# Performance work log

Hardware: AMD Instinct MI355X
Metric: run time of the kernel (lower is better)

## Reference

```python
import jax, jax.numpy as jnp
import numpy as np

BETA = 0.25
K = 1024   # codebook_size
D = 64     # emb_dim


def setup_inputs() -> dict:
    key = jax.random.key(0)
    k1, k2 = jax.random.split(key)
    z_e = jax.random.normal(k1, (32, 64, 64, D), dtype=jnp.float32)
    codebook = jax.random.normal(k2, (K, D), dtype=jnp.float32) * 0.05
    return {"z_e": z_e, "codebook": codebook}


def reference(z_e, codebook):
    sg = jax.lax.stop_gradient
    k, d = codebook.shape
    z = z_e.reshape(-1, d)                                   # [N, D]
    # squared euclidean distances: ||z||^2 + ||e||^2 - 2 z.e
    z_sq = jnp.sum(z * z, axis=1, keepdims=True)             # [N, 1]
    e_sq = jnp.sum(codebook * codebook, axis=1)              # [K]
    distances = z_sq + e_sq[None, :] - 2.0 * (z @ codebook.T)  # [N, K]
    indices = jnp.argmin(distances, axis=1)                  # [N] int
    z_q = jnp.take(codebook, indices, axis=0).reshape(z_e.shape)
    commitment = jnp.mean((sg(z_e) - z_q) ** 2)
    codebook_loss = jnp.mean((z_e - sg(z_q)) ** 2)
    z_q_st = z_e + sg(z_q - z_e)
    loss_vq = codebook_loss + BETA * commitment
    # perplexity (no-grad in original)
    n = z.shape[0]
    counts = jnp.zeros((k,), dtype=jnp.float32).at[indices].add(1.0)
    avg_probs = sg(counts / n)
    perplexity = jnp.exp(-jnp.sum(avg_probs * jnp.log(avg_probs + 1e-12)))
    return z_q_st, indices.reshape(z_e.shape[:-1]), loss_vq, perplexity
```

## Files before the change

kernel.cpp:

```cpp
#include <hip/hip_runtime.h>

#define N_VEC   131072
#define D       64
#define KCODES  1024
#define NT      64
#define BLK     256
#define VPB     128
#define CH      4
#define NCH     (NT / CH)

typedef __attribute__((ext_vector_type(8))) short bf16x8;
typedef __attribute__((ext_vector_type(4))) float f32x4;

#define GLD16(dst, src) __builtin_amdgcn_global_load_lds(                      \
    (const __attribute__((address_space(1))) void*)(src),                      \
    (__attribute__((address_space(3))) void*)(dst), 16, 0, 0)


__device__ __forceinline__ float4 f4fma(float4 a, float4 b, float4 c) {
    return make_float4(fmaf(a.x, b.x, c.x), fmaf(a.y, b.y, c.y),
                       fmaf(a.z, b.z, c.z), fmaf(a.w, b.w, c.w));
}
__device__ __forceinline__ float f4rsum(float4 a) {
    return (a.x + a.y) + (a.z + a.w);
}
__device__ __forceinline__ unsigned short f2bf(float f) {
    union { float f; unsigned u; } x; x.f = f;
    unsigned r = x.u + 0x7FFFu + ((x.u >> 16) & 1u);
    return (unsigned short)(r >> 16);
}
__device__ __forceinline__ float bf2f(unsigned short h) {
    union { unsigned u; float f; } x; x.u = ((unsigned)h) << 16;
    return x.f;
}
__device__ __forceinline__ int   f_as_i(float f) { union { float f; int i; } x; x.f = f; return x.i; }
__device__ __forceinline__ float i_as_f(int i)   { union { int i; float f; } x; x.i = i; return x.f; }

__global__ void prep_kernel(const float* __restrict__ cb, float* __restrict__ esq,
                            bf16x8* __restrict__ afrag, float4* __restrict__ efrag) {
    __shared__ float sesq[64];
    const int tid = threadIdx.x;
    const int c0  = blockIdx.x * 64;
    if (tid < 64) {
        const float4* c4 = reinterpret_cast<const float4*>(cb + (size_t)(c0 + tid) * D);
        float4 p = make_float4(0.f, 0.f, 0.f, 0.f);
        #pragma unroll
        for (int i = 0; i < 16; ++i) { float4 v = c4[i]; p = f4fma(v, v, p); }
        float e = f4rsum(p);
        esq[c0 + tid] = e;
        sesq[tid] = e;
    }
    __syncthreads();
    const int tt = tid >> 6;
    const int L  = tid & 63;
    const int t  = blockIdx.x * 4 + tt;
    const int g  = L >> 4;
    const int r  = t * 16 + (L & 15);
    #pragma unroll
    for (int ks = 0; ks < 2; ++ks) {
        const float* src = cb + (size_t)r * D + ks * 32 + g * 8;
        bf16x8 h, l;
        #pragma unroll
        for (int e = 0; e < 8; ++e) {
            float f = src[e];
            unsigned short hb = f2bf(f);
            float lo = f - bf2f(hb);
            h[e] = (short)hb;
            l[e] = (short)f2bf(lo);
        }
        afrag[(t * 4 + ks * 2 + 0) * 64 + L] = h;
        afrag[(t * 4 + ks * 2 + 1) * 64 + L] = l;
    }
    float4 ef;
    ef.x = sesq[tt * 16 + g * 4 + 0];
    ef.y = sesq[tt * 16 + g * 4 + 1];
    ef.z = sesq[tt * 16 + g * 4 + 2];
    ef.w = sesq[tt * 16 + g * 4 + 3];
    efrag[t * 64 + L] = ef;
}

__device__ __forceinline__ void insd(float ov, int og,
                                     float& v0, float& v1, float& v2,
                                     int& g0, int& g1, int& g2) {
    bool b1 = (ov > v0) || (ov == v0 && og < g0);
    bool b2 = (ov > v1) || (ov == v1 && og < g1);
    bool b3 = (ov > v2) || (ov == v2 && og < g2);
    float nv2 = b2 ? v1 : (b3 ? ov : v2);
    int   ng2 = b2 ? g1 : (b3 ? og : g2);
    float nv1 = b1 ? v0 : (b2 ? ov : v1);
    int   ng1 = b1 ? g0 : (b2 ? og : g1);
    v0 = b1 ? ov : v0;
    g0 = b1 ? og : g0;
    v1 = nv1; g1 = ng1; v2 = nv2; g2 = ng2;
}

__launch_bounds__(BLK)
__global__ void vq_fused(const float* __restrict__ z_e, const float* __restrict__ cb,
                         const float* __restrict__ esq,
                         const float4* __restrict__ afrag4, const float4* __restrict__ efrag,
                         float* __restrict__ zq_out, float* __restrict__ idx_out,
                         float* __restrict__ sse, int* __restrict__ counts) {
    __shared__ float4 scb[2][CH * 4 * 64];
    __shared__ float4 sef[2][CH * 64];
    char* ovl = (char*)&scb[0][0];
    int  (*scand)[3] = reinterpret_cast<int(*)[3]>(ovl);
    float* sZsq = reinterpret_cast<float*>(ovl + 2048);
    float* sS1  = reinterpret_cast<float*>(ovl + 2560);
    float* sS2  = reinterpret_cast<float*>(ovl + 3072);
    float* sC2  = reinterpret_cast<float*>(ovl + 3584);
    float* sred = reinterpret_cast<float*>(ovl + 4096);

    const int tid  = threadIdx.x;
    const int wave = tid >> 6;
    const int L    = tid & 63;
    const int lrow = L & 15;
    const int g    = L >> 4;
    const size_t vbase = (size_t)blockIdx.x * VPB + wave * 32;

    bf16x8 zhi[2][2], zlo[2][2];
    #pragma unroll
    for (int b = 0; b < 2; ++b) {
        #pragma unroll
        for (int ks = 0; ks < 2; ++ks) {
            const float* zp = z_e + (vbase + b * 16 + lrow) * D + ks * 32 + g * 8;
            float4 u0 = *reinterpret_cast<const float4*>(zp);
            float4 u1 = *reinterpret_cast<const float4*>(zp + 4);
            float fv[8] = {u0.x, u0.y, u0.z, u0.w, u1.x, u1.y, u1.z, u1.w};
            bf16x8 h, l;
            #pragma unroll
            for (int e = 0; e < 8; ++e) {
                unsigned short hb = f2bf(fv[e]);
                float lo = fv[e] - bf2f(hb);
                h[e] = (short)hb;
                l[e] = (short)f2bf(lo);
            }
            zhi[b][ks] = h; zlo[b][ks] = l;
        }
    }

    float m1[2], m2[2], m3[2];
    #pragma unroll
    for (int b = 0; b < 2; ++b) { m1[b] = m2[b] = m3[b] = -INFINITY; }

    #pragma unroll
    for (int i = 0; i < 4; ++i) GLD16(&scb[0][i * BLK + tid], afrag4 + i * BLK + tid);
    GLD16(&sef[0][tid], efrag + tid);

    int cur = 0;
    for (int c = 0; c < NCH; ++c) {
        __syncthreads();
        if (c + 1 < NCH) {
            const float4* gA = afrag4 + (size_t)(c + 1) * (CH * 4 * 64);
            const float4* gE = efrag + (size_t)(c + 1) * (CH * 64);
            #pragma unroll
            for (int i = 0; i < 4; ++i) GLD16(&scb[cur ^ 1][i * BLK + tid], gA + i * BLK + tid);
            GLD16(&sef[cur ^ 1][tid], gE + tid);
        }

        #pragma unroll
        for (int tt = 0; tt < CH; ++tt) {
            const int tglob = c * CH + tt;
            const bf16x8* fr = reinterpret_cast<const bf16x8*>(&scb[cur][tt * 256]);
            bf16x8 Ah0 = fr[0 * 64 + L];
            bf16x8 Al0 = fr[1 * 64 + L];
            bf16x8 Ah1 = fr[2 * 64 + L];
            bf16x8 Al1 = fr[3 * 64 + L];
            float4 ef  = sef[cur][tt * 64 + L];

            #pragma unroll
            for (int b = 0; b < 2; ++b) {
                f32x4 aA = (f32x4){0.f, 0.f, 0.f, 0.f};
                f32x4 aB = (f32x4){0.f, 0.f, 0.f, 0.f};
                aA = __builtin_amdgcn_mfma_f32_16x16x32_bf16(Ah0, zhi[b][0], aA, 0, 0, 0);
                aB = __builtin_amdgcn_mfma_f32_16x16x32_bf16(Ah0, zlo[b][0], aB, 0, 0, 0);
                aB = __builtin_amdgcn_mfma_f32_16x16x32_bf16(Al0, zhi[b][0], aB, 0, 0, 0);
                aA = __builtin_amdgcn_mfma_f32_16x16x32_bf16(Ah1, zhi[b][1], aA, 0, 0, 0);
                aB = __builtin_amdgcn_mfma_f32_16x16x32_bf16(Ah1, zlo[b][1], aB, 0, 0, 0);
                aB = __builtin_amdgcn_mfma_f32_16x16x32_bf16(Al1, zhi[b][1], aB, 0, 0, 0);

                #pragma unroll
                for (int j = 0; j < 4; ++j) {
                    float ej = (j == 0) ? ef.x : (j == 1) ? ef.y : (j == 2) ? ef.z : ef.w;
                    float s = fmaf(2.0f, aA[j], fmaf(2.0f, aB[j], -ej));
                    int komp = 255 - ((tglob << 2) | j);
                    float pd = i_as_f((f_as_i(s) & 0xFFFFFF00) | komp);
                    float t1 = fminf(m1[b], pd); m1[b] = fmaxf(m1[b], pd);
                    float t2 = fminf(m2[b], t1); m2[b] = fmaxf(m2[b], t1);
                    m3[b] = fmaxf(m3[b], t2);
                }
            }
        }
        cur ^= 1;
    }

    __syncthreads();

    #pragma unroll
    for (int b = 0; b < 2; ++b) {
        float v0, v1, v2; int g0, g1, g2;
        {
            int p0 = f_as_i(m1[b]), p1 = f_as_i(m2[b]), p2 = f_as_i(m3[b]);
            int c0 = 255 - (p0 & 255), c1 = 255 - (p1 & 255), c2 = 255 - (p2 & 255);
            v0 = i_as_f(p0 & ~255); g0 = (c0 >> 2) * 16 + g * 4 + (c0 & 3);
            v1 = i_as_f(p1 & ~255); g1 = (c1 >> 2) * 16 + g * 4 + (c1 & 3);
            v2 = i_as_f(p2 & ~255); g2 = (c2 >> 2) * 16 + g * 4 + (c2 & 3);
        }
        #pragma unroll
        for (int m = 16; m <= 32; m <<= 1) {
            float ov0 = __shfl_xor(v0, m), ov1 = __shfl_xor(v1, m), ov2 = __shfl_xor(v2, m);
            int   og0 = __shfl_xor(g0, m), og1 = __shfl_xor(g1, m), og2 = __shfl_xor(g2, m);
            insd(ov0, og0, v0, v1, v2, g0, g1, g2);
            insd(ov1, og1, v0, v1, v2, g0, g1, g2);
            insd(ov2, og2, v0, v1, v2, g0, g1, g2);
        }
        if (g == 0) {
            int lv = wave * 32 + b * 16 + lrow;
            scand[lv][0] = g0; scand[lv][1] = g1; scand[lv][2] = g2;
        }
    }
    __syncthreads();

    const int vid = tid & (VPB - 1);
    const int sub = tid >> 7;
    const size_t n = (size_t)blockIdx.x * VPB + vid;
    {
        const float4* z4 = reinterpret_cast<const float4*>(z_e + n * D);
        if (sub == 0) {
            int ci0 = scand[vid][0];
            const float4* cp0 = reinterpret_cast<const float4*>(cb + (size_t)ci0 * D);
            float4 pq = make_float4(0.f, 0.f, 0.f, 0.f);
            float4 s0 = pq;
            #pragma unroll
            for (int i = 0; i < 16; ++i) {
                float4 zz = z4[i];
                pq = f4fma(zz, zz, pq);
                s0 = f4fma(zz, cp0[i], s0);
            }
            sZsq[vid] = f4rsum(pq);
            sS1[vid]  = f4rsum(s0);
        } else {
            int ci1 = scand[vid][1];
            int ci2 = scand[vid][2];
            const float4* cp1 = reinterpret_cast<const float4*>(cb + (size_t)ci1 * D);
            const float4* cp2 = reinterpret_cast<const float4*>(cb + (size_t)ci2 * D);
            float4 s1 = make_float4(0.f, 0.f, 0.f, 0.f);
            float4 s2 = s1;
            #pragma unroll
            for (int i = 0; i < 16; ++i) {
                float4 zz = z4[i];
                s1 = f4fma(zz, cp1[i], s1);
                s2 = f4fma(zz, cp2[i], s2);
            }
            sS2[vid] = f4rsum(s1);
            sC2[vid] = f4rsum(s2);
        }
    }
    __syncthreads();

    float v = 0.f;
    if (sub == 0) {
        int ci0 = scand[vid][0], ci1 = scand[vid][1], ci2 = scand[vid][2];
        float zsq = sZsq[vid];
        float d0 = fmaf(-2.0f, sS1[vid], zsq + esq[ci0]);
        float d1 = fmaf(-2.0f, sS2[vid], zsq + esq[ci1]);
        float d2 = fmaf(-2.0f, sC2[vid], zsq + esq[ci2]);
        float bd = d0; int bi = ci0;
        if (d1 < bd || (d1 == bd && ci1 < bi)) { bd = d1; bi = ci1; }
        if (d2 < bd || (d2 == bd && ci2 < bi)) { bd = d2; bi = ci2; }
        idx_out[n] = (float)bi;
        atomicAdd(&counts[bi], 1);
        scand[vid][0] = bi;
        v = bd;
    }
    #pragma unroll
    for (int off = 32; off > 0; off >>= 1) v += __shfl_down(v, off);
    if ((tid & 63) == 0) sred[tid >> 6] = v;
    __syncthreads();
    if (tid == 0) atomicAdd(sse, (sred[0] + sred[1]) + (sred[2] + sred[3]));

    const float4* cb4 = reinterpret_cast<const float4*>(cb);
    float4* zq4 = reinterpret_cast<float4*>(zq_out) + (size_t)blockIdx.x * (VPB * 16);
    #pragma unroll
    for (int i = 0; i < 8; ++i) {
        int mi  = i * BLK + tid;
        int vec = mi >> 4;
        int e   = mi & 15;
        zq4[mi] = cb4[(size_t)scand[vec][0] * 16 + e];
    }
}

__global__ void finalize_kernel(const int* __restrict__ counts, const float* __restrict__ sse,
                                float* __restrict__ out_loss, float* __restrict__ out_perp) {
    __shared__ float red[256];
    int tid = threadIdx.x;
    float hsum = 0.f;
    for (int k = tid; k < KCODES; k += 256) {
        float p = (float)counts[k] / (float)N_VEC;
        hsum += p * logf(p + 1e-12f);
    }
    red[tid] = hsum;
    __syncthreads();
    for (int s = 128; s > 0; s >>= 1) {
        if (tid < s) red[tid] += red[tid + s];
        __syncthreads();
    }
    if (tid == 0) {
        out_loss[0] = 1.25f * sse[0] / 8388608.0f;
        out_perp[0] = expf(-red[0]);
    }
}

extern "C" void kernel_launch(void* const* d_in, const int* in_sizes, int n_in,
                              void* d_out, int out_size, void* d_ws, size_t ws_size,
                              hipStream_t stream) {
    const float* z_e = (const float*)d_in[0];
    const float* cb  = (const float*)d_in[1];

    float* out  = (float*)d_out;
    float* zq   = out;
    float* idxo = out + (size_t)N_VEC * D;
    float* loss = idxo + N_VEC;
    float* perp = loss + 1;

    char* ws = (char*)d_ws;
    int*    counts = (int*)ws;
    float*  sse    = (float*)(ws + 4096);
    float*  esq    = (float*)(ws + 5120);
    float4* efrag  = (float4*)(ws + 16384);
    bf16x8* afrag  = (bf16x8*)(ws + 81920);

    hipMemsetAsync(d_ws, 0, 5120, stream);
    prep_kernel<<<16, 256, 0, stream>>>(cb, esq, afrag, efrag);
    vq_fused<<<N_VEC / VPB, BLK, 0, stream>>>(z_e, cb, esq, (const float4*)afrag, efrag,
                                              zq, idxo, sse, counts);
    finalize_kernel<<<1, 256, 0, stream>>>(counts, sse, loss, perp);
}
```

Baseline: 106.0 us.

## Load codebook fragments directly from global into registers with prefetch, drop LDS staging

```diff
diff --git a/kernel.cpp b/kernel.cpp
--- a/kernel.cpp
+++ b/kernel.cpp
@@ -6,15 +6,9 @@
 #define NT      64
 #define BLK     256
 #define VPB     128
-#define CH      4
-#define NCH     (NT / CH)
 
 typedef __attribute__((ext_vector_type(8))) short bf16x8;
 typedef __attribute__((ext_vector_type(4))) float f32x4;
-
-#define GLD16(dst, src) __builtin_amdgcn_global_load_lds(                      \
-    (const __attribute__((address_space(1))) void*)(src),                      \
-    (__attribute__((address_space(3))) void*)(dst), 16, 0, 0)
 
 
 __device__ __forceinline__ float4 f4fma(float4 a, float4 b, float4 c) {
@@ -97,18 +91,15 @@
 __launch_bounds__(BLK)
 __global__ void vq_fused(const float* __restrict__ z_e, const float* __restrict__ cb,
                          const float* __restrict__ esq,
-                         const float4* __restrict__ afrag4, const float4* __restrict__ efrag,
+                         const bf16x8* __restrict__ afragv, const float4* __restrict__ efrag,
                          float* __restrict__ zq_out, float* __restrict__ idx_out,
                          float* __restrict__ sse, int* __restrict__ counts) {
-    __shared__ float4 scb[2][CH * 4 * 64];
-    __shared__ float4 sef[2][CH * 64];
-    char* ovl = (char*)&scb[0][0];
-    int  (*scand)[3] = reinterpret_cast<int(*)[3]>(ovl);
-    float* sZsq = reinterpret_cast<float*>(ovl + 2048);
-    float* sS1  = reinterpret_cast<float*>(ovl + 2560);
-    float* sS2  = reinterpret_cast<float*>(ovl + 3072);
-    float* sC2  = reinterpret_cast<float*>(ovl + 3584);
-    float* sred = reinterpret_cast<float*>(ovl + 4096);
+    __shared__ int   scand[VPB][3];
+    __shared__ float sZsq[VPB];
+    __shared__ float sS1[VPB];
+    __shared__ float sS2[VPB];
+    __shared__ float sC2[VPB];
+    __shared__ float sred[4];
 
     const int tid  = threadIdx.x;
     const int wave = tid >> 6;
@@ -142,58 +133,48 @@
     #pragma unroll
     for (int b = 0; b < 2; ++b) { m1[b] = m2[b] = m3[b] = -INFINITY; }
 
-    #pragma unroll
-    for (int i = 0; i < 4; ++i) GLD16(&scb[0][i * BLK + tid], afrag4 + i * BLK + tid);
-    GLD16(&sef[0][tid], efrag + tid);
-
-    int cur = 0;
-    for (int c = 0; c < NCH; ++c) {
-        __syncthreads();
-        if (c + 1 < NCH) {
-            const float4* gA = afrag4 + (size_t)(c + 1) * (CH * 4 * 64);
-            const float4* gE = efrag + (size_t)(c + 1) * (CH * 64);
+    bf16x8 nAh0 = afragv[0 * 64 + L];
+    bf16x8 nAl0 = afragv[1 * 64 + L];
+    bf16x8 nAh1 = afragv[2 * 64 + L];
+    bf16x8 nAl1 = afragv[3 * 64 + L];
+    float4 nef  = efrag[L];
+
+    #pragma unroll 2
+    for (int t = 0; t < NT; ++t) {
+        bf16x8 Ah0 = nAh0, Al0 = nAl0, Ah1 = nAh1, Al1 = nAl1;
+        float4 ef  = nef;
+        if (t + 1 < NT) {
+            const bf16x8* np = afragv + (size_t)(t + 1) * 256;
+            nAh0 = np[0 * 64 + L];
+            nAl0 = np[1 * 64 + L];
+            nAh1 = np[2 * 64 + L];
+            nAl1 = np[3 * 64 + L];
+            nef  = efrag[(size_t)(t + 1) * 64 + L];
+        }
+
+        #pragma unroll
+        for (int b = 0; b < 2; ++b) {
+            f32x4 aA = (f32x4){0.f, 0.f, 0.f, 0.f};
+            f32x4 aB = (f32x4){0.f, 0.f, 0.f, 0.f};
+            aA = __builtin_amdgcn_mfma_f32_16x16x32_bf16(Ah0, zhi[b][0], aA, 0, 0, 0);
+            aB = __builtin_amdgcn_mfma_f32_16x16x32_bf16(Ah0, zlo[b][0], aB, 0, 0, 0);
+            aB = __builtin_amdgcn_mfma_f32_16x16x32_bf16(Al0, zhi[b][0], aB, 0, 0, 0);
+            aA = __builtin_amdgcn_mfma_f32_16x16x32_bf16(Ah1, zhi[b][1], aA, 0, 0, 0);
+            aB = __builtin_amdgcn_mfma_f32_16x16x32_bf16(Ah1, zlo[b][1], aB, 0, 0, 0);
+            aB = __builtin_amdgcn_mfma_f32_16x16x32_bf16(Al1, zhi[b][1], aB, 0, 0, 0);
+
             #pragma unroll
-            for (int i = 0; i < 4; ++i) GLD16(&scb[cur ^ 1][i * BLK + tid], gA + i * BLK + tid);
-            GLD16(&sef[cur ^ 1][tid], gE + tid);
-        }
-
-        #pragma unroll
-        for (int tt = 0; tt < CH; ++tt) {
-            const int tglob = c * CH + tt;
-            const bf16x8* fr = reinterpret_cast<const bf16x8*>(&scb[cur][tt * 256]);
-            bf16x8 Ah0 = fr[0 * 64 + L];
-            bf16x8 Al0 = fr[1 * 64 + L];
-            bf16x8 Ah1 = fr[2 * 64 + L];
-            bf16x8 Al1 = fr[3 * 64 + L];
-            float4 ef  = sef[cur][tt * 64 + L];
-
-            #pragma unroll
-            for (int b = 0; b < 2; ++b) {
-                f32x4 aA = (f32x4){0.f, 0.f, 0.f, 0.f};
-                f32x4 aB = (f32x4){0.f, 0.f, 0.f, 0.f};
-                aA = __builtin_amdgcn_mfma_f32_16x16x32_bf16(Ah0, zhi[b][0], aA, 0, 0, 0);
-                aB = __builtin_amdgcn_mfma_f32_16x16x32_bf16(Ah0, zlo[b][0], aB, 0, 0, 0);
-                aB = __builtin_amdgcn_mfma_f32_16x16x32_bf16(Al0, zhi[b][0], aB, 0, 0, 0);
-                aA = __builtin_amdgcn_mfma_f32_16x16x32_bf16(Ah1, zhi[b][1], aA, 0, 0, 0);
-                aB = __builtin_amdgcn_mfma_f32_16x16x32_bf16(Ah1, zlo[b][1], aB, 0, 0, 0);
-                aB = __builtin_amdgcn_mfma_f32_16x16x32_bf16(Al1, zhi[b][1], aB, 0, 0, 0);
-
-                #pragma unroll
-                for (int j = 0; j < 4; ++j) {
-                    float ej = (j == 0) ? ef.x : (j == 1) ? ef.y : (j == 2) ? ef.z : ef.w;
-                    float s = fmaf(2.0f, aA[j], fmaf(2.0f, aB[j], -ej));
-                    int komp = 255 - ((tglob << 2) | j);
-                    float pd = i_as_f((f_as_i(s) & 0xFFFFFF00) | komp);
-                    float t1 = fminf(m1[b], pd); m1[b] = fmaxf(m1[b], pd);
-                    float t2 = fminf(m2[b], t1); m2[b] = fmaxf(m2[b], t1);
-                    m3[b] = fmaxf(m3[b], t2);
-                }
+            for (int j = 0; j < 4; ++j) {
+                float ej = (j == 0) ? ef.x : (j == 1) ? ef.y : (j == 2) ? ef.z : ef.w;
+                float s = fmaf(2.0f, aA[j], fmaf(2.0f, aB[j], -ej));
+                int komp = 255 - ((t << 2) | j);
+                float pd = i_as_f((f_as_i(s) & 0xFFFFFF00) | komp);
+                float t1 = fminf(m1[b], pd); m1[b] = fmaxf(m1[b], pd);
+                float t2 = fminf(m2[b], t1); m2[b] = fmaxf(m2[b], t1);
+                m3[b] = fmaxf(m3[b], t2);
             }
         }
-        cur ^= 1;
-    }
-
-    __syncthreads();
+    }
 
     #pragma unroll
     for (int b = 0; b < 2; ++b) {
@@ -331,7 +312,7 @@
 
     hipMemsetAsync(d_ws, 0, 5120, stream);
     prep_kernel<<<16, 256, 0, stream>>>(cb, esq, afrag, efrag);
-    vq_fused<<<N_VEC / VPB, BLK, 0, stream>>>(z_e, cb, esq, (const float4*)afrag, efrag,
+    vq_fused<<<N_VEC / VPB, BLK, 0, stream>>>(z_e, cb, esq, afrag, efrag,
                                               zq, idxo, sse, counts);
     finalize_kernel<<<1, 256, 0, stream>>>(counts, sse, loss, perp);
 }
```

New measurement: 112.0 us. 5.6% more time.
